# Optimization experiments

Hardware: AMD Instinct MI355X
Metric: run time of the kernel (lower is better)

The kernel has to match this reference:

```python
import jax, jax.numpy as jnp
import numpy as np

N = 50000
E = 1600000
INDIM, HIDIM, OUTDIM = 256, 128, 64


def setup_inputs() -> dict:
    key = jax.random.key(0)
    ks = jax.random.split(key, 4)
    x = jax.random.normal(ks[0], (N, INDIM), dtype=jnp.float32)
    edge_index = jax.random.randint(ks[1], (2, E), 0, N, dtype=jnp.int32)
    W1 = jax.random.normal(ks[2], (INDIM, HIDIM), dtype=jnp.float32) / np.float32(np.sqrt(INDIM))
    b1 = jnp.zeros((HIDIM,), dtype=jnp.float32)
    W2 = jax.random.normal(ks[3], (HIDIM, OUTDIM), dtype=jnp.float32) / np.float32(np.sqrt(HIDIM))
    b2 = jnp.zeros((OUTDIM,), dtype=jnp.float32)
    return {"x": x, "edge_index": edge_index, "W1": W1, "b1": b1, "W2": W2, "b2": b2}


def _gcn_conv(x, row, col, norm, W, b):
    # PyG GCNConv: transform first, then normalized scatter-add aggregation, then bias
    h = x @ W                              # [N, out]
    msg = h[row] * norm[:, None]           # gather source features, scale by edge norm
    out = jax.ops.segment_sum(msg, col, num_segments=x.shape[0])  # scatter-add to dst
    return out + b


def reference(x, edge_index, W1, b1, W2, b2):
    n = x.shape[0]
    # add self loops (PyG default add_self_loops=True)
    loops = jnp.arange(n, dtype=edge_index.dtype)
    row = jnp.concatenate([edge_index[0], loops])  # source nodes
    col = jnp.concatenate([edge_index[1], loops])  # destination nodes
    # symmetric normalization: deg^{-1/2}[row] * deg^{-1/2}[col], deg over dst incl. self loops
    deg = jax.ops.segment_sum(jnp.ones_like(col, dtype=x.dtype), col, num_segments=n)
    dinv = jnp.where(deg > 0, jax.lax.rsqrt(jnp.maximum(deg, 1.0)), 0.0)
    norm = dinv[row] * dinv[col]
    h = jax.nn.relu(_gcn_conv(x, row, col, norm, W1, b1))
    return _gcn_conv(h, row, col, norm, W2, b2)
```

## Files before the change

kernel.cpp:

```cpp
#include <hip/hip_runtime.h>

#define NN 50000
#define NE 1600000
#define INDIM 256
#define HIDIM 128
#define OUTDIM 64

#define NRANGE 64
#define RSPAN 800
#define ACAP 32768
#define NBBLK 1563

typedef unsigned int uint;
typedef unsigned long long ull;
typedef unsigned short ushort;
typedef __attribute__((ext_vector_type(8))) short bf16x8;
typedef __attribute__((ext_vector_type(4))) float f32x4;

__device__ __forceinline__ ushort f2bf(float f) {
    uint u = __float_as_uint(f);
    uint r = (u + 0x7FFFu + ((u >> 16) & 1u)) >> 16;
    return (ushort)r;
}
__device__ __forceinline__ uint pk2(float a, float b) {
    return (uint)f2bf(a) | ((uint)f2bf(b) << 16);
}
__device__ __forceinline__ float bf_lo(uint u) { return __uint_as_float(u << 16); }
__device__ __forceinline__ float bf_hi(uint u) { return __uint_as_float(u & 0xFFFF0000u); }

#define ACC8(u) do { \
    a0 += bf_lo((u).x); a1 += bf_hi((u).x); \
    a2 += bf_lo((u).y); a3 += bf_hi((u).y); \
    a4 += bf_lo((u).z); a5 += bf_hi((u).z); \
    a6 += bf_lo((u).w); a7 += bf_hi((u).w); \
} while (0)


__global__ void k_wt(const float* __restrict__ W1, const float* __restrict__ W2,
                     ushort* __restrict__ W1T, ushort* __restrict__ W2T) {
    int idx = blockIdx.x * 256 + threadIdx.x;
    if (idx < INDIM * HIDIM) {
        int k = idx / HIDIM, nn = idx % HIDIM;
        W1T[nn * INDIM + k] = f2bf(W1[idx]);
    } else {
        int j = idx - INDIM * HIDIM;
        if (j < HIDIM * OUTDIM) {
            int k = j / OUTDIM, nn = j % OUTDIM;
            W2T[nn * HIDIM + k] = f2bf(W2[j]);
        }
    }
}


__global__ void k_bcnt(const int* __restrict__ col, int* __restrict__ bcnt) {
    __shared__ int bins[NRANGE];
    int tid = threadIdx.x;
    if (tid < NRANGE) bins[tid] = 0;
    __syncthreads();
    int base = blockIdx.x * 1024 + tid;
#pragma unroll
    for (int k = 0; k < 4; k++) {
        int i = base + k * 256;
        if (i < NE) atomicAdd(&bins[col[i] / RSPAN], 1);
    }
    __syncthreads();
    if (tid < NRANGE) bcnt[tid * NBBLK + blockIdx.x] = bins[tid];
}


__global__ void k_bscan(const int* __restrict__ bcnt, int* __restrict__ bbase,
                        int* __restrict__ rcur) {
    __shared__ int wsum[16];
    __shared__ int woff[16];
    int r = blockIdx.x;
    const int* src = bcnt + r * NBBLK;
    int* dst = bbase + r * NBBLK;
    int tid = threadIdx.x, lane = tid & 63, wid = tid >> 6;
    int seg = tid * 2;
    int l0 = (seg < NBBLK) ? src[seg] : 0;
    int l1 = (seg + 1 < NBBLK) ? src[seg + 1] : 0;
    int sum = l0 + l1;
    int incl = sum;
#pragma unroll
    for (int off = 1; off < 64; off <<= 1) {
        int t = __shfl_up(incl, off);
        if (lane >= off) incl += t;
    }
    if (lane == 63) wsum[wid] = incl;
    __syncthreads();
    if (wid == 0 && lane < 16) {
        int wv = wsum[lane];
        int wincl = wv;
#pragma unroll
        for (int off = 1; off < 16; off <<= 1) {
            int t = __shfl_up(wincl, off);
            if (lane >= off) wincl += t;
        }
        woff[lane] = wincl - wv;
    }
    __syncthreads();
    int run = incl - sum + woff[wid];
    if (seg < NBBLK) dst[seg] = run;
    if (seg + 1 < NBBLK) dst[seg + 1] = run + l0;
    if (tid == 1023) rcur[r] = run + sum;
}


__global__ void k_bscat(const int* __restrict__ row, const int* __restrict__ col,
                        const int* __restrict__ bbase, uint* __restrict__ staged) {
    __shared__ int cur[NRANGE];
    int tid = threadIdx.x;
    if (tid < NRANGE) cur[tid] = bbase[tid * NBBLK + blockIdx.x];
    __syncthreads();
    int base = blockIdx.x * 1024 + tid;
#pragma unroll
    for (int k = 0; k < 4; k++) {
        int i = base + k * 256;
        if (i < NE) {
            int d = col[i], s = row[i];
            int r = d / RSPAN;
            int off = atomicAdd(&cur[r], 1);
            staged[(size_t)r * ACAP + off] = ((uint)s << 10) | (uint)(d - r * RSPAN);
        }
    }
}


__global__ void k_sort(const uint* __restrict__ staged, const int* __restrict__ rcur,
                       int* __restrict__ row_ptr, float* __restrict__ dinv,
                       ushort* __restrict__ ssrc) {
    __shared__ int bins[RSPAN];
    __shared__ int wsum[16];
    __shared__ int woff[16];
    int r = blockIdx.x;
    int tid = threadIdx.x, lane = tid & 63, wid = tid >> 6;
    int lo = r * RSPAN;
    int count = rcur[r];
    int base = 0;
    for (int rr = 0; rr < r; rr++) base += rcur[rr];
    const uint* st = staged + (size_t)r * ACAP;

    if (tid < RSPAN) bins[tid] = 0;
    __syncthreads();

    for (int i = tid; i < count; i += 1024)
        atomicAdd(&bins[st[i] & 1023u], 1);
    __syncthreads();

    int v = (tid < RSPAN) ? bins[tid] : 0;
    int incl = v;
#pragma unroll
    for (int off = 1; off < 64; off <<= 1) {
        int t = __shfl_up(incl, off);
        if (lane >= off) incl += t;
    }
    if (lane == 63) wsum[wid] = incl;
    __syncthreads();
    if (wid == 0 && lane < 16) {
        int wv = wsum[lane];
        int wincl = wv;
#pragma unroll
        for (int off = 1; off < 16; off <<= 1) {
            int t = __shfl_up(wincl, off);
            if (lane >= off) wincl += t;
        }
        woff[lane] = wincl - wv;
    }
    __syncthreads();
    int excl = incl - v + woff[wid];
    int idx = lo + tid;
    if (tid < RSPAN && idx <= NN) {
        if (idx < NN) {
            row_ptr[idx] = base + excl;
            dinv[idx] = rsqrtf((float)(v + 1));
        } else {
            row_ptr[NN] = base + excl;
        }
    }
    __syncthreads();
    if (tid < RSPAN) bins[tid] = base + excl;
    __syncthreads();

    for (int i = tid; i < count; i += 1024) {
        uint rec = st[i];
        int pos = atomicAdd(&bins[rec & 1023u], 1);
        ssrc[pos] = (ushort)(rec >> 10);
    }
}


__global__ void k_gemm1(const float* __restrict__ A, const ushort* __restrict__ W1T,
                        const float* __restrict__ dinv, ushort* __restrict__ g1s, int n) {
    __shared__ ushort As[64 * 40];
    __shared__ ushort Bs[128 * 40];
    int tid = threadIdx.x;
    int w = tid >> 6, lane = tid & 63;
    int ln = lane & 15, quad = lane >> 4;
    int row0 = blockIdx.x * 64;
    int n0 = w * 32;

    f32x4 acc[4][2];
#pragma unroll
    for (int m = 0; m < 4; m++)
#pragma unroll
        for (int t = 0; t < 2; t++) acc[m][t] = (f32x4){0.f, 0.f, 0.f, 0.f};

    int ar = tid >> 2;
    int ac = (tid & 3) * 8;

    for (int k0 = 0; k0 < INDIM; k0 += 32) {
        {
            int gr = row0 + ar;
            uint4 u = make_uint4(0, 0, 0, 0);
            if (gr < n) {
                const float* p = A + (size_t)gr * INDIM + k0 + ac;
                float4 v0 = *(const float4*)p;
                float4 v1 = *(const float4*)(p + 4);
                u.x = pk2(v0.x, v0.y); u.y = pk2(v0.z, v0.w);
                u.z = pk2(v1.x, v1.y); u.w = pk2(v1.z, v1.w);
            }
            *(uint4*)(As + ar * 40 + ac) = u;
        }
#pragma unroll
        for (int it = 0; it < 2; it++) {
            int idx = tid + it * 256;
            int bn = idx >> 2, bc = (idx & 3) * 8;
            uint4 u = *(const uint4*)(W1T + (size_t)bn * INDIM + k0 + bc);
            *(uint4*)(Bs + bn * 40 + bc) = u;
        }
        __syncthreads();

        bf16x8 af[4], bf[2];
#pragma unroll
        for (int m = 0; m < 4; m++)
            af[m] = *(const bf16x8*)(As + (m * 16 + ln) * 40 + quad * 8);
#pragma unroll
        for (int t = 0; t < 2; t++)
            bf[t] = *(const bf16x8*)(Bs + (n0 + t * 16 + ln) * 40 + quad * 8);
#pragma unroll
        for (int m = 0; m < 4; m++)
#pragma unroll
            for (int t = 0; t < 2; t++)
                acc[m][t] = __builtin_amdgcn_mfma_f32_16x16x32_bf16(af[m], bf[t], acc[m][t], 0, 0, 0);
        __syncthreads();
    }

    int slice = w >> 1;
    int fbase = (w & 1) * 32;
#pragma unroll
    for (int m = 0; m < 4; m++) {
#pragma unroll
        for (int r = 0; r < 4; r++) {
            int gr = row0 + m * 16 + quad * 4 + r;
            if (gr < n) {
                float dv = dinv[gr];
#pragma unroll
                for (int t = 0; t < 2; t++) {
                    int cj = t * 16 + ln;
                    g1s[((size_t)slice * NN + gr) * 64 + fbase + cj] = f2bf(acc[m][t][r] * dv);
                }
            }
        }
    }
}


__global__ void k_agg1(const ushort* __restrict__ g1s, const float* __restrict__ dinv,
                       const int* __restrict__ row_ptr, const ushort* __restrict__ ssrc,
                       const float* __restrict__ b1, ushort* __restrict__ hrb) {
    int slice = blockIdx.x & 1;
    int dbase = (blockIdx.x >> 1) * 32;
    int wid = threadIdx.x >> 6, lane = threadIdx.x & 63;
    int grp = lane >> 3, fl = lane & 7;
    int d = dbase + wid * 8 + grp;
    if (d >= NN) return;
    const ushort* gs = g1s + (size_t)slice * NN * 64 + fl * 8;
    float a0 = 0.f, a1 = 0.f, a2 = 0.f, a3 = 0.f;
    float a4 = 0.f, a5 = 0.f, a6 = 0.f, a7 = 0.f;
    int e0 = row_ptr[d], e1 = row_ptr[d + 1];
    if (e1 > e0) {
        int last = e1 - 1;
        int sB0 = ssrc[min(e0 + 0, last)];
        int sB1 = ssrc[min(e0 + 1, last)];
        int sB2 = ssrc[min(e0 + 2, last)];
        int sB3 = ssrc[min(e0 + 3, last)];
        uint4 uA0 = *(const uint4*)(gs + (size_t)sB0 * 64);
        uint4 uA1 = *(const uint4*)(gs + (size_t)sB1 * 64);
        uint4 uA2 = *(const uint4*)(gs + (size_t)sB2 * 64);
        uint4 uA3 = *(const uint4*)(gs + (size_t)sB3 * 64);
        sB0 = ssrc[min(e0 + 4, last)];
        sB1 = ssrc[min(e0 + 5, last)];
        sB2 = ssrc[min(e0 + 6, last)];
        sB3 = ssrc[min(e0 + 7, last)];
        for (int eb = e0; eb < e1; eb += 4) {
            int p0 = ssrc[min(eb + 8, last)];
            int p1 = ssrc[min(eb + 9, last)];
            int p2 = ssrc[min(eb + 10, last)];
            int p3 = ssrc[min(eb + 11, last)];
            uint4 v0 = *(const uint4*)(gs + (size_t)sB0 * 64);
            uint4 v1 = *(const uint4*)(gs + (size_t)sB1 * 64);
            uint4 v2 = *(const uint4*)(gs + (size_t)sB2 * 64);
            uint4 v3 = *(const uint4*)(gs + (size_t)sB3 * 64);
            uint4 z = make_uint4(0u, 0u, 0u, 0u);
            if (eb + 1 >= e1) uA1 = z;
            if (eb + 2 >= e1) uA2 = z;
            if (eb + 3 >= e1) uA3 = z;
            ACC8(uA0); ACC8(uA1); ACC8(uA2); ACC8(uA3);
            uA0 = v0; uA1 = v1; uA2 = v2; uA3 = v3;
            sB0 = p0; sB1 = p1; sB2 = p2; sB3 = p3;
        }
    }
    uint4 ud = *(const uint4*)(gs + (size_t)d * 64);
    ACC8(ud);
    float dv = dinv[d];
    const float* bp = b1 + slice * 64 + fl * 8;
    float4 bb0 = *(const float4*)bp;
    float4 bb1 = *(const float4*)(bp + 4);
    uint4 o;
    o.x = pk2(fmaxf(a0 * dv + bb0.x, 0.f), fmaxf(a1 * dv + bb0.y, 0.f));
    o.y = pk2(fmaxf(a2 * dv + bb0.z, 0.f), fmaxf(a3 * dv + bb0.w, 0.f));
    o.z = pk2(fmaxf(a4 * dv + bb1.x, 0.f), fmaxf(a5 * dv + bb1.y, 0.f));
    o.w = pk2(fmaxf(a6 * dv + bb1.z, 0.f), fmaxf(a7 * dv + bb1.w, 0.f));
    *(uint4*)(hrb + ((size_t)slice * NN + d) * 64 + fl * 8) = o;
}


__global__ void k_gemm2(const ushort* __restrict__ hrb, const ushort* __restrict__ W2T,
                        const float* __restrict__ dinv, ushort* __restrict__ g2s, int n) {
    __shared__ ushort As[64 * 40];
    __shared__ ushort Bs[64 * 40];
    int tid = threadIdx.x;
    int w = tid >> 6, lane = tid & 63;
    int ln = lane & 15, quad = lane >> 4;
    int row0 = blockIdx.x * 64;
    int n0 = w * 16;

    f32x4 acc[4];
#pragma unroll
    for (int m = 0; m < 4; m++) acc[m] = (f32x4){0.f, 0.f, 0.f, 0.f};

    int ar = tid >> 2;
    int ac = (tid & 3) * 8;

    for (int k0 = 0; k0 < HIDIM; k0 += 32) {
        {
            int gr = row0 + ar;
            uint4 u = make_uint4(0, 0, 0, 0);
            if (gr < n) u = *(const uint4*)(hrb + ((size_t)(k0 >> 6) * NN + gr) * 64 + (k0 & 63) + ac);
            *(uint4*)(As + ar * 40 + ac) = u;
        }
        {
            int bn = tid >> 2, bc = (tid & 3) * 8;
            uint4 u = *(const uint4*)(W2T + (size_t)bn * HIDIM + k0 + bc);
            *(uint4*)(Bs + bn * 40 + bc) = u;
        }
        __syncthreads();

        bf16x8 bf = *(const bf16x8*)(Bs + (n0 + ln) * 40 + quad * 8);
#pragma unroll
        for (int m = 0; m < 4; m++) {
            bf16x8 af = *(const bf16x8*)(As + (m * 16 + ln) * 40 + quad * 8);
            acc[m] = __builtin_amdgcn_mfma_f32_16x16x32_bf16(af, bf, acc[m], 0, 0, 0);
        }
        __syncthreads();
    }

    int col = n0 + ln;
#pragma unroll
    for (int m = 0; m < 4; m++) {
#pragma unroll
        for (int r = 0; r < 4; r++) {
            int gr = row0 + m * 16 + quad * 4 + r;
            if (gr < n) {
                g2s[(size_t)gr * 64 + col] = f2bf(acc[m][r] * dinv[gr]);
            }
        }
    }
}


__global__ void k_agg2(const ushort* __restrict__ g2s, const float* __restrict__ dinv,
                       const int* __restrict__ row_ptr, const ushort* __restrict__ ssrc,
                       const float* __restrict__ b2, float* __restrict__ out) {
    int dbase = blockIdx.x * 32;
    int wid = threadIdx.x >> 6, lane = threadIdx.x & 63;
    int grp = lane >> 3, fl = lane & 7;
    int d = dbase + wid * 8 + grp;
    if (d >= NN) return;
    const ushort* gs = g2s + fl * 8;
    float a0 = 0.f, a1 = 0.f, a2 = 0.f, a3 = 0.f;
    float a4 = 0.f, a5 = 0.f, a6 = 0.f, a7 = 0.f;
    int e0 = row_ptr[d], e1 = row_ptr[d + 1];
    if (e1 > e0) {
        int last = e1 - 1;
        int sB0 = ssrc[min(e0 + 0, last)];
        int sB1 = ssrc[min(e0 + 1, last)];
        int sB2 = ssrc[min(e0 + 2, last)];
        int sB3 = ssrc[min(e0 + 3, last)];
        uint4 uA0 = *(const uint4*)(gs + (size_t)sB0 * 64);
        uint4 uA1 = *(const uint4*)(gs + (size_t)sB1 * 64);
        uint4 uA2 = *(const uint4*)(gs + (size_t)sB2 * 64);
        uint4 uA3 = *(const uint4*)(gs + (size_t)sB3 * 64);
        sB0 = ssrc[min(e0 + 4, last)];
        sB1 = ssrc[min(e0 + 5, last)];
        sB2 = ssrc[min(e0 + 6, last)];
        sB3 = ssrc[min(e0 + 7, last)];
        for (int eb = e0; eb < e1; eb += 4) {
            int p0 = ssrc[min(eb + 8, last)];
            int p1 = ssrc[min(eb + 9, last)];
            int p2 = ssrc[min(eb + 10, last)];
            int p3 = ssrc[min(eb + 11, last)];
            uint4 v0 = *(const uint4*)(gs + (size_t)sB0 * 64);
            uint4 v1 = *(const uint4*)(gs + (size_t)sB1 * 64);
            uint4 v2 = *(const uint4*)(gs + (size_t)sB2 * 64);
            uint4 v3 = *(const uint4*)(gs + (size_t)sB3 * 64);
            uint4 z = make_uint4(0u, 0u, 0u, 0u);
            if (eb + 1 >= e1) uA1 = z;
            if (eb + 2 >= e1) uA2 = z;
            if (eb + 3 >= e1) uA3 = z;
            ACC8(uA0); ACC8(uA1); ACC8(uA2); ACC8(uA3);
            uA0 = v0; uA1 = v1; uA2 = v2; uA3 = v3;
            sB0 = p0; sB1 = p1; sB2 = p2; sB3 = p3;
        }
    }
    uint4 ud = *(const uint4*)(gs + (size_t)d * 64);
    ACC8(ud);
    float dv = dinv[d];
    const float* bp = b2 + fl * 8;
    float4 bb0 = *(const float4*)bp;
    float4 bb1 = *(const float4*)(bp + 4);
    float4 r0, r1;
    r0.x = a0 * dv + bb0.x;
    r0.y = a1 * dv + bb0.y;
    r0.z = a2 * dv + bb0.z;
    r0.w = a3 * dv + bb0.w;
    r1.x = a4 * dv + bb1.x;
    r1.y = a5 * dv + bb1.y;
    r1.z = a6 * dv + bb1.z;
    r1.w = a7 * dv + bb1.w;
    float* op = out + (size_t)d * OUTDIM + fl * 8;
    *(float4*)op = r0;
    *(float4*)(op + 4) = r1;
}


extern "C" void kernel_launch(void* const* d_in, const int* in_sizes, int n_in,
                              void* d_out, int out_size, void* d_ws, size_t ws_size,
                              hipStream_t stream) {
    const float* x   = (const float*)d_in[0];
    const int*   ei  = (const int*)d_in[1];
    const float* W1  = (const float*)d_in[2];
    const float* b1  = (const float*)d_in[3];
    const float* W2  = (const float*)d_in[4];
    const float* b2  = (const float*)d_in[5];
    float* out = (float*)d_out;

    const int* row = ei;
    const int* col = ei + NE;

    size_t off = 0;
    auto alloc = [&](size_t bytes) {
        void* p = (char*)d_ws + off;
        off += (bytes + 255) & ~(size_t)255;
        return p;
    };
    float*  dinv     = (float*) alloc((size_t)NN * 4);
    int*    row_ptr  = (int*)   alloc((size_t)(NN + 1) * 4);
    int*    rcur     = (int*)   alloc(NRANGE * 4);
    int*    bcnt     = (int*)   alloc((size_t)NRANGE * NBBLK * 4);
    int*    bbase    = (int*)   alloc((size_t)NRANGE * NBBLK * 4);
    uint*   staged   = (uint*)  alloc((size_t)NRANGE * ACAP * 4);
    ushort* ssrc     = (ushort*)alloc((size_t)NE * 2);
    ushort* W1T      = (ushort*)alloc((size_t)INDIM * HIDIM * 2);
    ushort* W2T      = (ushort*)alloc((size_t)HIDIM * OUTDIM * 2);
    ushort* g1s      = (ushort*)alloc((size_t)NN * HIDIM * 2);
    ushort* hrb      = (ushort*)alloc((size_t)NN * HIDIM * 2);
    ushort* g2s      = (ushort*)alloc((size_t)NN * OUTDIM * 2);

    const int nb32 = (NN + 31) / 32;
    const int nb64 = (NN + 63) / 64;

    k_wt<<<(INDIM * HIDIM + HIDIM * OUTDIM + 255) / 256, 256, 0, stream>>>(W1, W2, W1T, W2T);

    k_bcnt<<<NBBLK, 256, 0, stream>>>(col, bcnt);
    k_bscan<<<NRANGE, 1024, 0, stream>>>(bcnt, bbase, rcur);
    k_bscat<<<NBBLK, 256, 0, stream>>>(row, col, bbase, staged);

    k_sort<<<NRANGE, 1024, 0, stream>>>(staged, rcur, row_ptr, dinv, ssrc);

    k_gemm1<<<nb64, 256, 0, stream>>>(x, W1T, dinv, g1s, NN);
    k_agg1<<<nb32 * 2, 256, 0, stream>>>(g1s, dinv, row_ptr, ssrc, b1, hrb);
    k_gemm2<<<nb64, 256, 0, stream>>>(hrb, W2T, dinv, g2s, NN);
    k_agg2<<<nb32, 256, 0, stream>>>(g2s, dinv, row_ptr, ssrc, b2, out);
}
```

Before: 222.0 us.

## Sort destination nodes by degree and split features into 32-wide slices

Builds a degree histogram during the CSR sort, scans it, and scatters nodes into a degree-sorted permutation. The aggregation kernels walk nodes through this permutation so lanes in a wavefront see similar edge counts and diverge less. Intermediate features are re-laid out into 32-column slices, so each node uses 4 lanes per slice instead of 8, and agg2 now splits into two slices. This adds two small kernels and an extra perm indirection, and it loses the spatial locality of writing outputs in node order.

```diff
diff --git a/kernel.cpp b/kernel.cpp
--- a/kernel.cpp
+++ b/kernel.cpp
@@ -10,6 +10,7 @@
 #define RSPAN 800
 #define ACAP 32768
 #define NBBLK 1563
+#define NDEG 256
 
 typedef unsigned int uint;
 typedef unsigned long long ull;
@@ -52,9 +53,11 @@
 }
 
 
-__global__ void k_bcnt(const int* __restrict__ col, int* __restrict__ bcnt) {
+__global__ void k_bcnt(const int* __restrict__ col, int* __restrict__ bcnt,
+                       int* __restrict__ dhist) {
     __shared__ int bins[NRANGE];
     int tid = threadIdx.x;
+    if (blockIdx.x == 0) dhist[tid] = 0;
     if (tid < NRANGE) bins[tid] = 0;
     __syncthreads();
     int base = blockIdx.x * 1024 + tid;
@@ -128,10 +131,11 @@
 
 __global__ void k_sort(const uint* __restrict__ staged, const int* __restrict__ rcur,
                        int* __restrict__ row_ptr, float* __restrict__ dinv,
-                       ushort* __restrict__ ssrc) {
+                       ushort* __restrict__ ssrc, int* __restrict__ dhist) {
     __shared__ int bins[RSPAN];
     __shared__ int wsum[16];
     __shared__ int woff[16];
+    __shared__ int dh[NDEG];
     int r = blockIdx.x;
     int tid = threadIdx.x, lane = tid & 63, wid = tid >> 6;
     int lo = r * RSPAN;
@@ -141,6 +145,7 @@
     const uint* st = staged + (size_t)r * ACAP;
 
     if (tid < RSPAN) bins[tid] = 0;
+    if (tid < NDEG) dh[tid] = 0;
     __syncthreads();
 
     for (int i = tid; i < count; i += 1024)
@@ -173,6 +178,7 @@
         if (idx < NN) {
             row_ptr[idx] = base + excl;
             dinv[idx] = rsqrtf((float)(v + 1));
+            atomicAdd(&dh[min(v, NDEG - 1)], 1);
         } else {
             row_ptr[NN] = base + excl;
         }
@@ -180,11 +186,41 @@
     __syncthreads();
     if (tid < RSPAN) bins[tid] = base + excl;
     __syncthreads();
+    if (tid < NDEG && dh[tid]) atomicAdd(&dhist[tid], dh[tid]);
 
     for (int i = tid; i < count; i += 1024) {
         uint rec = st[i];
         int pos = atomicAdd(&bins[rec & 1023u], 1);
         ssrc[pos] = (ushort)(rec >> 10);
+    }
+}
+
+
+__global__ void k_dscan(const int* __restrict__ dhist, int* __restrict__ dcur) {
+    int lane = threadIdx.x;
+    int b = lane * 4;
+    int v0 = dhist[b], v1 = dhist[b + 1], v2 = dhist[b + 2], v3 = dhist[b + 3];
+    int s = v0 + v1 + v2 + v3;
+    int incl = s;
+#pragma unroll
+    for (int off = 1; off < 64; off <<= 1) {
+        int t = __shfl_up(incl, off);
+        if (lane >= off) incl += t;
+    }
+    int excl = incl - s;
+    dcur[b] = excl;
+    dcur[b + 1] = excl + v0;
+    dcur[b + 2] = excl + v0 + v1;
+    dcur[b + 3] = excl + v0 + v1 + v2;
+}
+
+__global__ void k_dscat(const int* __restrict__ row_ptr, int* __restrict__ dcur,
+                        int* __restrict__ perm) {
+    int d = blockIdx.x * 256 + threadIdx.x;
+    if (d < NN) {
+        int deg = row_ptr[d + 1] - row_ptr[d];
+        int pos = atomicAdd(&dcur[min(deg, NDEG - 1)], 1);
+        perm[pos] = d;
     }
 }
 
@@ -245,8 +281,6 @@
         __syncthreads();
     }
 
-    int slice = w >> 1;
-    int fbase = (w & 1) * 32;
 #pragma unroll
     for (int m = 0; m < 4; m++) {
 #pragma unroll
@@ -257,7 +291,7 @@
 #pragma unroll
                 for (int t = 0; t < 2; t++) {
                     int cj = t * 16 + ln;
-                    g1s[((size_t)slice * NN + gr) * 64 + fbase + cj] = f2bf(acc[m][t][r] * dv);
+                    g1s[((size_t)w * NN + gr) * 32 + cj] = f2bf(acc[m][t][r] * dv);
                 }
             }
         }
@@ -267,14 +301,16 @@
 
 __global__ void k_agg1(const ushort* __restrict__ g1s, const float* __restrict__ dinv,
                        const int* __restrict__ row_ptr, const ushort* __restrict__ ssrc,
-                       const float* __restrict__ b1, ushort* __restrict__ hrb) {
-    int slice = blockIdx.x & 1;
-    int dbase = (blockIdx.x >> 1) * 32;
+                       const int* __restrict__ perm, const float* __restrict__ b1,
+                       ushort* __restrict__ hrb) {
+    int slice = blockIdx.x & 3;
+    int dbase = (blockIdx.x >> 2) * 64;
     int wid = threadIdx.x >> 6, lane = threadIdx.x & 63;
-    int grp = lane >> 3, fl = lane & 7;
-    int d = dbase + wid * 8 + grp;
-    if (d >= NN) return;
-    const ushort* gs = g1s + (size_t)slice * NN * 64 + fl * 8;
+    int grp = lane >> 2, fl = lane & 3;
+    int di = dbase + wid * 16 + grp;
+    if (di >= NN) return;
+    int d = perm[di];
+    const ushort* gs = g1s + (size_t)slice * NN * 32 + fl * 8;
     float a0 = 0.f, a1 = 0.f, a2 = 0.f, a3 = 0.f;
     float a4 = 0.f, a5 = 0.f, a6 = 0.f, a7 = 0.f;
     int e0 = row_ptr[d], e1 = row_ptr[d + 1];
@@ -284,10 +320,10 @@
         int sB1 = ssrc[min(e0 + 1, last)];
         int sB2 = ssrc[min(e0 + 2, last)];
         int sB3 = ssrc[min(e0 + 3, last)];
-        uint4 uA0 = *(const uint4*)(gs + (size_t)sB0 * 64);
-        uint4 uA1 = *(const uint4*)(gs + (size_t)sB1 * 64);
-        uint4 uA2 = *(const uint4*)(gs + (size_t)sB2 * 64);
-        uint4 uA3 = *(const uint4*)(gs + (size_t)sB3 * 64);
+        uint4 uA0 = *(const uint4*)(gs + (size_t)sB0 * 32);
+        uint4 uA1 = *(const uint4*)(gs + (size_t)sB1 * 32);
+        uint4 uA2 = *(const uint4*)(gs + (size_t)sB2 * 32);
+        uint4 uA3 = *(const uint4*)(gs + (size_t)sB3 * 32);
         sB0 = ssrc[min(e0 + 4, last)];
         sB1 = ssrc[min(e0 + 5, last)];
         sB2 = ssrc[min(e0 + 6, last)];
@@ -297,10 +333,10 @@
             int p1 = ssrc[min(eb + 9, last)];
             int p2 = ssrc[min(eb + 10, last)];
             int p3 = ssrc[min(eb + 11, last)];
-            uint4 v0 = *(const uint4*)(gs + (size_t)sB0 * 64);
-            uint4 v1 = *(const uint4*)(gs + (size_t)sB1 * 64);
-            uint4 v2 = *(const uint4*)(gs + (size_t)sB2 * 64);
-            uint4 v3 = *(const uint4*)(gs + (size_t)sB3 * 64);
+            uint4 v0 = *(const uint4*)(gs + (size_t)sB0 * 32);
+            uint4 v1 = *(const uint4*)(gs + (size_t)sB1 * 32);
+            uint4 v2 = *(const uint4*)(gs + (size_t)sB2 * 32);
+            uint4 v3 = *(const uint4*)(gs + (size_t)sB3 * 32);
             uint4 z = make_uint4(0u, 0u, 0u, 0u);
             if (eb + 1 >= e1) uA1 = z;
             if (eb + 2 >= e1) uA2 = z;
@@ -310,10 +346,10 @@
             sB0 = p0; sB1 = p1; sB2 = p2; sB3 = p3;
         }
     }
-    uint4 ud = *(const uint4*)(gs + (size_t)d * 64);
+    uint4 ud = *(const uint4*)(gs + (size_t)d * 32);
     ACC8(ud);
     float dv = dinv[d];
-    const float* bp = b1 + slice * 64 + fl * 8;
+    const float* bp = b1 + slice * 32 + fl * 8;
     float4 bb0 = *(const float4*)bp;
     float4 bb1 = *(const float4*)(bp + 4);
     uint4 o;
@@ -321,7 +357,7 @@
     o.y = pk2(fmaxf(a2 * dv + bb0.z, 0.f), fmaxf(a3 * dv + bb0.w, 0.f));
     o.z = pk2(fmaxf(a4 * dv + bb1.x, 0.f), fmaxf(a5 * dv + bb1.y, 0.f));
     o.w = pk2(fmaxf(a6 * dv + bb1.z, 0.f), fmaxf(a7 * dv + bb1.w, 0.f));
-    *(uint4*)(hrb + ((size_t)slice * NN + d) * 64 + fl * 8) = o;
+    *(uint4*)(hrb + ((size_t)slice * NN + d) * 32 + fl * 8) = o;
 }
 
 
@@ -343,10 +379,11 @@
     int ac = (tid & 3) * 8;
 
     for (int k0 = 0; k0 < HIDIM; k0 += 32) {
+        int hs = k0 >> 5;
         {
             int gr = row0 + ar;
             uint4 u = make_uint4(0, 0, 0, 0);
-            if (gr < n) u = *(const uint4*)(hrb + ((size_t)(k0 >> 6) * NN + gr) * 64 + (k0 & 63) + ac);
+            if (gr < n) u = *(const uint4*)(hrb + ((size_t)hs * NN + gr) * 32 + ac);
             *(uint4*)(As + ar * 40 + ac) = u;
         }
         {
@@ -366,13 +403,14 @@
     }
 
     int col = n0 + ln;
+    int s2 = col >> 5, cj = col & 31;
 #pragma unroll
     for (int m = 0; m < 4; m++) {
 #pragma unroll
         for (int r = 0; r < 4; r++) {
             int gr = row0 + m * 16 + quad * 4 + r;
             if (gr < n) {
-                g2s[(size_t)gr * 64 + col] = f2bf(acc[m][r] * dinv[gr]);
+                g2s[((size_t)s2 * NN + gr) * 32 + cj] = f2bf(acc[m][r] * dinv[gr]);
             }
         }
     }
@@ -381,13 +419,16 @@
 
 __global__ void k_agg2(const ushort* __restrict__ g2s, const float* __restrict__ dinv,
                        const int* __restrict__ row_ptr, const ushort* __restrict__ ssrc,
-                       const float* __restrict__ b2, float* __restrict__ out) {
-    int dbase = blockIdx.x * 32;
+                       const int* __restrict__ perm, const float* __restrict__ b2,
+                       float* __restrict__ out) {
+    int slice = blockIdx.x & 1;
+    int dbase = (blockIdx.x >> 1) * 64;
     int wid = threadIdx.x >> 6, lane = threadIdx.x & 63;
-    int grp = lane >> 3, fl = lane & 7;
-    int d = dbase + wid * 8 + grp;
-    if (d >= NN) return;
-    const ushort* gs = g2s + fl * 8;
+    int grp = lane >> 2, fl = lane & 3;
+    int di = dbase + wid * 16 + grp;
+    if (di >= NN) return;
+    int d = perm[di];
+    const ushort* gs = g2s + (size_t)slice * NN * 32 + fl * 8;
     float a0 = 0.f, a1 = 0.f, a2 = 0.f, a3 = 0.f;
     float a4 = 0.f, a5 = 0.f, a6 = 0.f, a7 = 0.f;
     int e0 = row_ptr[d], e1 = row_ptr[d + 1];
@@ -397,10 +438,10 @@
         int sB1 = ssrc[min(e0 + 1, last)];
         int sB2 = ssrc[min(e0 + 2, last)];
         int sB3 = ssrc[min(e0 + 3, last)];
-        uint4 uA0 = *(const uint4*)(gs + (size_t)sB0 * 64);
-        uint4 uA1 = *(const uint4*)(gs + (size_t)sB1 * 64);
-        uint4 uA2 = *(const uint4*)(gs + (size_t)sB2 * 64);
-        uint4 uA3 = *(const uint4*)(gs + (size_t)sB3 * 64);
+        uint4 uA0 = *(const uint4*)(gs + (size_t)sB0 * 32);
+        uint4 uA1 = *(const uint4*)(gs + (size_t)sB1 * 32);
+        uint4 uA2 = *(const uint4*)(gs + (size_t)sB2 * 32);
+        uint4 uA3 = *(const uint4*)(gs + (size_t)sB3 * 32);
         sB0 = ssrc[min(e0 + 4, last)];
         sB1 = ssrc[min(e0 + 5, last)];
         sB2 = ssrc[min(e0 + 6, last)];
@@ -410,10 +451,10 @@
             int p1 = ssrc[min(eb + 9, last)];
             int p2 = ssrc[min(eb + 10, last)];
             int p3 = ssrc[min(eb + 11, last)];
-            uint4 v0 = *(const uint4*)(gs + (size_t)sB0 * 64);
-            uint4 v1 = *(const uint4*)(gs + (size_t)sB1 * 64);
-            uint4 v2 = *(const uint4*)(gs + (size_t)sB2 * 64);
-            uint4 v3 = *(const uint4*)(gs + (size_t)sB3 * 64);
+            uint4 v0 = *(const uint4*)(gs + (size_t)sB0 * 32);
+            uint4 v1 = *(const uint4*)(gs + (size_t)sB1 * 32);
+            uint4 v2 = *(const uint4*)(gs + (size_t)sB2 * 32);
+            uint4 v3 = *(const uint4*)(gs + (size_t)sB3 * 32);
             uint4 z = make_uint4(0u, 0u, 0u, 0u);
             if (eb + 1 >= e1) uA1 = z;
             if (eb + 2 >= e1) uA2 = z;
@@ -423,10 +464,10 @@
             sB0 = p0; sB1 = p1; sB2 = p2; sB3 = p3;
         }
     }
-    uint4 ud = *(const uint4*)(gs + (size_t)d * 64);
+    uint4 ud = *(const uint4*)(gs + (size_t)d * 32);
     ACC8(ud);
     float dv = dinv[d];
-    const float* bp = b2 + fl * 8;
+    const float* bp = b2 + slice * 32 + fl * 8;
     float4 bb0 = *(const float4*)bp;
     float4 bb1 = *(const float4*)(bp + 4);
     float4 r0, r1;
@@ -438,7 +479,7 @@
     r1.y = a5 * dv + bb1.y;
     r1.z = a6 * dv + bb1.z;
     r1.w = a7 * dv + bb1.w;
-    float* op = out + (size_t)d * OUTDIM + fl * 8;
+    float* op = out + (size_t)d * OUTDIM + slice * 32 + fl * 8;
     *(float4*)op = r0;
     *(float4*)(op + 4) = r1;
 }
@@ -476,20 +517,25 @@
     ushort* g1s      = (ushort*)alloc((size_t)NN * HIDIM * 2);
     ushort* hrb      = (ushort*)alloc((size_t)NN * HIDIM * 2);
     ushort* g2s      = (ushort*)alloc((size_t)NN * OUTDIM * 2);
-
-    const int nb32 = (NN + 31) / 32;
+    int*    dhist    = (int*)   alloc((size_t)NDEG * 4);
+    int*    dcur     = (int*)   alloc((size_t)NDEG * 4);
+    int*    perm     = (int*)   alloc((size_t)NN * 4);
+
     const int nb64 = (NN + 63) / 64;
 
     k_wt<<<(INDIM * HIDIM + HIDIM * OUTDIM + 255) / 256, 256, 0, stream>>>(W1, W2, W1T, W2T);
 
-    k_bcnt<<<NBBLK, 256, 0, stream>>>(col, bcnt);
+    k_bcnt<<<NBBLK, 256, 0, stream>>>(col, bcnt, dhist);
     k_bscan<<<NRANGE, 1024, 0, stream>>>(bcnt, bbase, rcur);
     k_bscat<<<NBBLK, 256, 0, stream>>>(row, col, bbase, staged);
 
-    k_sort<<<NRANGE, 1024, 0, stream>>>(staged, rcur, row_ptr, dinv, ssrc);
+    k_sort<<<NRANGE, 1024, 0, stream>>>(staged, rcur, row_ptr, dinv, ssrc, dhist);
+
+    k_dscan<<<1, 64, 0, stream>>>(dhist, dcur);
+    k_dscat<<<(NN + 255) / 256, 256, 0, stream>>>(row_ptr, dcur, perm);
 
     k_gemm1<<<nb64, 256, 0, stream>>>(x, W1T, dinv, g1s, NN);
-    k_agg1<<<nb32 * 2, 256, 0, stream>>>(g1s, dinv, row_ptr, ssrc, b1, hrb);
+    k_agg1<<<nb64 * 4, 256, 0, stream>>>(g1s, dinv, row_ptr, ssrc, perm, b1, hrb);
     k_gemm2<<<nb64, 256, 0, stream>>>(hrb, W2T, dinv, g2s, NN);
-    k_agg2<<<nb32, 256, 0, stream>>>(g2s, dinv, row_ptr, ssrc, b2, out);
-}
+    k_agg2<<<nb64 * 2, 256, 0, stream>>>(g2s, dinv, row_ptr, ssrc, perm, b2, out);
+}
```

New measurement: 343.7 us. 54.8% more time.

## Sort destination nodes by degree for balanced aggregation and split sort into more ranges

Applied to the files above, without the earlier changes.

Builds a degree histogram during the CSR sort, scans it, and scatters node ids into a degree-ordered permutation. The aggregation kernels then process nodes in that order, so lanes in a wavefront have similar edge counts and divergence is reduced. It also doubles the number of sort ranges (halving span and staging capacity) to give the sort kernel more blocks. This adds two small kernels, an extra indirection, and less locality in output writes.

```diff
diff --git a/kernel.cpp b/kernel.cpp
--- a/kernel.cpp
+++ b/kernel.cpp
@@ -6,10 +6,11 @@
 #define HIDIM 128
 #define OUTDIM 64
 
-#define NRANGE 64
-#define RSPAN 800
-#define ACAP 32768
+#define NRANGE 128
+#define RSPAN 400
+#define ACAP 16384
 #define NBBLK 1563
+#define NDEG 256
 
 typedef unsigned int uint;
 typedef unsigned long long ull;
@@ -52,9 +53,11 @@
 }
 
 
-__global__ void k_bcnt(const int* __restrict__ col, int* __restrict__ bcnt) {
+__global__ void k_bcnt(const int* __restrict__ col, int* __restrict__ bcnt,
+                       int* __restrict__ dhist) {
     __shared__ int bins[NRANGE];
     int tid = threadIdx.x;
+    if (blockIdx.x == 0) dhist[tid] = 0;
     if (tid < NRANGE) bins[tid] = 0;
     __syncthreads();
     int base = blockIdx.x * 1024 + tid;
@@ -128,10 +131,11 @@
 
 __global__ void k_sort(const uint* __restrict__ staged, const int* __restrict__ rcur,
                        int* __restrict__ row_ptr, float* __restrict__ dinv,
-                       ushort* __restrict__ ssrc) {
+                       ushort* __restrict__ ssrc, int* __restrict__ dhist) {
     __shared__ int bins[RSPAN];
     __shared__ int wsum[16];
     __shared__ int woff[16];
+    __shared__ int dh[NDEG];
     int r = blockIdx.x;
     int tid = threadIdx.x, lane = tid & 63, wid = tid >> 6;
     int lo = r * RSPAN;
@@ -141,6 +145,7 @@
     const uint* st = staged + (size_t)r * ACAP;
 
     if (tid < RSPAN) bins[tid] = 0;
+    if (tid < NDEG) dh[tid] = 0;
     __syncthreads();
 
     for (int i = tid; i < count; i += 1024)
@@ -173,6 +178,7 @@
         if (idx < NN) {
             row_ptr[idx] = base + excl;
             dinv[idx] = rsqrtf((float)(v + 1));
+            atomicAdd(&dh[min(v, NDEG - 1)], 1);
         } else {
             row_ptr[NN] = base + excl;
         }
@@ -180,12 +186,53 @@
     __syncthreads();
     if (tid < RSPAN) bins[tid] = base + excl;
     __syncthreads();
+    if (tid < NDEG && dh[tid]) atomicAdd(&dhist[tid], dh[tid]);
 
     for (int i = tid; i < count; i += 1024) {
         uint rec = st[i];
         int pos = atomicAdd(&bins[rec & 1023u], 1);
         ssrc[pos] = (ushort)(rec >> 10);
     }
+}
+
+
+__global__ void k_dscan(const int* __restrict__ dhist, int* __restrict__ dcur) {
+    int lane = threadIdx.x;
+    int b = lane * 4;
+    int v0 = dhist[b], v1 = dhist[b + 1], v2 = dhist[b + 2], v3 = dhist[b + 3];
+    int s = v0 + v1 + v2 + v3;
+    int incl = s;
+#pragma unroll
+    for (int off = 1; off < 64; off <<= 1) {
+        int t = __shfl_up(incl, off);
+        if (lane >= off) incl += t;
+    }
+    int excl = incl - s;
+    dcur[b] = excl;
+    dcur[b + 1] = excl + v0;
+    dcur[b + 2] = excl + v0 + v1;
+    dcur[b + 3] = excl + v0 + v1 + v2;
+}
+
+
+__global__ void k_dscat(const int* __restrict__ row_ptr, int* __restrict__ dcur,
+                        int* __restrict__ perm) {
+    __shared__ int h[NDEG];
+    __shared__ int boff[NDEG];
+    int tid = threadIdx.x;
+    int d = blockIdx.x * 256 + tid;
+    h[tid] = 0;
+    __syncthreads();
+    int bin = 0, myoff = 0;
+    if (d < NN) {
+        int deg = row_ptr[d + 1] - row_ptr[d];
+        bin = min(deg, NDEG - 1);
+        myoff = atomicAdd(&h[bin], 1);
+    }
+    __syncthreads();
+    if (h[tid]) boff[tid] = atomicAdd(&dcur[tid], h[tid]);
+    __syncthreads();
+    if (d < NN) perm[boff[bin] + myoff] = d;
 }
 
 
@@ -267,13 +314,15 @@
 
 __global__ void k_agg1(const ushort* __restrict__ g1s, const float* __restrict__ dinv,
                        const int* __restrict__ row_ptr, const ushort* __restrict__ ssrc,
-                       const float* __restrict__ b1, ushort* __restrict__ hrb) {
+                       const int* __restrict__ perm, const float* __restrict__ b1,
+                       ushort* __restrict__ hrb) {
     int slice = blockIdx.x & 1;
     int dbase = (blockIdx.x >> 1) * 32;
     int wid = threadIdx.x >> 6, lane = threadIdx.x & 63;
     int grp = lane >> 3, fl = lane & 7;
-    int d = dbase + wid * 8 + grp;
-    if (d >= NN) return;
+    int di = dbase + wid * 8 + grp;
+    if (di >= NN) return;
+    int d = perm[di];
     const ushort* gs = g1s + (size_t)slice * NN * 64 + fl * 8;
     float a0 = 0.f, a1 = 0.f, a2 = 0.f, a3 = 0.f;
     float a4 = 0.f, a5 = 0.f, a6 = 0.f, a7 = 0.f;
@@ -381,12 +430,14 @@
 
 __global__ void k_agg2(const ushort* __restrict__ g2s, const float* __restrict__ dinv,
                        const int* __restrict__ row_ptr, const ushort* __restrict__ ssrc,
-                       const float* __restrict__ b2, float* __restrict__ out) {
+                       const int* __restrict__ perm, const float* __restrict__ b2,
+                       float* __restrict__ out) {
     int dbase = blockIdx.x * 32;
     int wid = threadIdx.x >> 6, lane = threadIdx.x & 63;
     int grp = lane >> 3, fl = lane & 7;
-    int d = dbase + wid * 8 + grp;
-    if (d >= NN) return;
+    int di = dbase + wid * 8 + grp;
+    if (di >= NN) return;
+    int d = perm[di];
     const ushort* gs = g2s + fl * 8;
     float a0 = 0.f, a1 = 0.f, a2 = 0.f, a3 = 0.f;
     float a4 = 0.f, a5 = 0.f, a6 = 0.f, a7 = 0.f;
@@ -476,20 +527,26 @@
     ushort* g1s      = (ushort*)alloc((size_t)NN * HIDIM * 2);
     ushort* hrb      = (ushort*)alloc((size_t)NN * HIDIM * 2);
     ushort* g2s      = (ushort*)alloc((size_t)NN * OUTDIM * 2);
+    int*    dhist    = (int*)   alloc((size_t)NDEG * 4);
+    int*    dcur     = (int*)   alloc((size_t)NDEG * 4);
+    int*    perm     = (int*)   alloc((size_t)NN * 4);
 
     const int nb32 = (NN + 31) / 32;
     const int nb64 = (NN + 63) / 64;
 
     k_wt<<<(INDIM * HIDIM + HIDIM * OUTDIM + 255) / 256, 256, 0, stream>>>(W1, W2, W1T, W2T);
 
-    k_bcnt<<<NBBLK, 256, 0, stream>>>(col, bcnt);
+    k_bcnt<<<NBBLK, 256, 0, stream>>>(col, bcnt, dhist);
     k_bscan<<<NRANGE, 1024, 0, stream>>>(bcnt, bbase, rcur);
     k_bscat<<<NBBLK, 256, 0, stream>>>(row, col, bbase, staged);
 
-    k_sort<<<NRANGE, 1024, 0, stream>>>(staged, rcur, row_ptr, dinv, ssrc);
+    k_sort<<<NRANGE, 1024, 0, stream>>>(staged, rcur, row_ptr, dinv, ssrc, dhist);
+
+    k_dscan<<<1, 64, 0, stream>>>(dhist, dcur);
+    k_dscat<<<(NN + 255) / 256, 256, 0, stream>>>(row_ptr, dcur, perm);
 
     k_gemm1<<<nb64, 256, 0, stream>>>(x, W1T, dinv, g1s, NN);
-    k_agg1<<<nb32 * 2, 256, 0, stream>>>(g1s, dinv, row_ptr, ssrc, b1, hrb);
+    k_agg1<<<nb32 * 2, 256, 0, stream>>>(g1s, dinv, row_ptr, ssrc, perm, b1, hrb);
     k_gemm2<<<nb64, 256, 0, stream>>>(hrb, W2T, dinv, g2s, NN);
-    k_agg2<<<nb32, 256, 0, stream>>>(g2s, dinv, row_ptr, ssrc, b2, out);
-}
+    k_agg2<<<nb32, 256, 0, stream>>>(g2s, dinv, row_ptr, ssrc, perm, b2, out);
+}
```

Measured after the change: 231.4 us. 1.04x slower.
